# Performance work log

Hardware: AMD Instinct MI355X
Metric: run time of the kernel (lower is better)

Reference implementation:

```python
import jax, jax.numpy as jnp
import numpy as np

B, N, D, S, ITERS = 32, 4096, 256, 7, 3
EPS_LN = 1e-5

def _ln(x, g, b):
    m = jnp.mean(x, axis=-1, keepdims=True)
    v = jnp.mean((x - m) ** 2, axis=-1, keepdims=True)
    return g * (x - m) * jax.lax.rsqrt(v + EPS_LN) + b

def setup_inputs() -> dict:
    key = jax.random.key(0)
    ks = jax.random.split(key, 16)
    w = lambda k, shape: (jax.random.normal(k, shape, jnp.float32) * 0.02)
    return {
        "inputs": jax.random.normal(ks[0], (B, N, D), jnp.float32),
        "noise": jax.random.normal(ks[1], (B, S, D), jnp.float32),
        "ln_in_g": jnp.ones((D,), jnp.float32), "ln_in_b": jnp.zeros((D,), jnp.float32),
        "ln_slots_g": jnp.ones((D,), jnp.float32), "ln_slots_b": jnp.zeros((D,), jnp.float32),
        "ln_mlp_g": jnp.ones((D,), jnp.float32), "ln_mlp_b": jnp.zeros((D,), jnp.float32),
        "slots_mu": w(ks[2], (1, 1, D)),
        "slots_sigma": jnp.ones((1, 1, D), jnp.float32),
        "wq": w(ks[3], (D, D)), "bq": jnp.zeros((D,), jnp.float32),
        "wk": w(ks[4], (D, D)), "bk": jnp.zeros((D,), jnp.float32),
        "wv": w(ks[5], (D, D)), "bv": jnp.zeros((D,), jnp.float32),
        "w_ih": w(ks[6], (3 * D, D)), "b_ih": jnp.zeros((3 * D,), jnp.float32),
        "w_hh": w(ks[7], (3 * D, D)), "b_hh": jnp.zeros((3 * D,), jnp.float32),
        "w1": w(ks[8], (2 * D, D)), "b1": jnp.zeros((2 * D,), jnp.float32),
        "w2": w(ks[9], (D, 2 * D)), "b2": jnp.zeros((D,), jnp.float32),
    }

def reference(inputs, noise, ln_in_g, ln_in_b, ln_slots_g, ln_slots_b, ln_mlp_g, ln_mlp_b,
              slots_mu, slots_sigma, wq, bq, wk, bk, wv, bv,
              w_ih, b_ih, w_hh, b_hh, w1, b1, w2, b2):
    x = _ln(inputs, ln_in_g, ln_in_b)                      # [B,N,D]
    sigma = jax.nn.softplus(slots_sigma)
    slots = slots_mu + sigma * noise                       # [B,S,D]
    k = x @ wk.T + bk                                      # [B,N,D]
    v = x @ wv.T + bv                                      # [B,N,D]
    scale = D ** -0.5
    attn = None
    for _ in range(ITERS):
        slots_prev = slots
        q = _ln(slots, ln_slots_g, ln_slots_b) @ wq.T + bq  # [B,S,D]
        logits = jnp.einsum('bsd,bnd->bsn', q, k) * scale   # [B,S,N]
        attn = jax.nn.softmax(logits, axis=1) + 1e-8        # softmax over slots
        attn = attn / jnp.sum(attn, axis=-1, keepdims=True)
        updates = jnp.einsum('bsn,bnd->bsd', attn, v)       # [B,S,D]
        # GRUCell(updates, slots_prev), torch gate order (r, z, n)
        gi = updates @ w_ih.T + b_ih                        # [B,S,3D]
        gh = slots_prev @ w_hh.T + b_hh
        i_r, i_z, i_n = jnp.split(gi, 3, axis=-1)
        h_r, h_z, h_n = jnp.split(gh, 3, axis=-1)
        r = jax.nn.sigmoid(i_r + h_r)
        z = jax.nn.sigmoid(i_z + h_z)
        n = jnp.tanh(i_n + r * h_n)
        slots = (1.0 - z) * n + z * slots_prev
        h = jax.nn.relu(_ln(slots, ln_mlp_g, ln_mlp_b) @ w1.T + b1)
        slots = slots + h @ w2.T + b2
    return slots, jnp.swapaxes(attn, 1, 2)                 # [B,S,D], [B,N,S]
```

## Files before the change

kernel.cpp:

```cpp
#include <hip/hip_runtime.h>
#include <stdint.h>

typedef unsigned short u16;
typedef unsigned int u32;
typedef float f32x4 __attribute__((ext_vector_type(4)));
typedef short short8 __attribute__((ext_vector_type(8)));

#define NBAT 32
#define NSEQ 4096
#define ND 256
#define NSLOT 7
#define NCHUNK 64

__device__ __forceinline__ u32 bf16rne(float f){
  u32 u = __float_as_uint(f);
  u = u + 0x7FFFu + ((u >> 16) & 1u);
  return u >> 16;
}
__device__ __forceinline__ u32 packbf(float a, float b){
  return (bf16rne(a) & 0xFFFFu) | (bf16rne(b) << 16);
}
__device__ __forceinline__ float bflo(u32 u){ return __uint_as_float(u << 16); }
__device__ __forceinline__ float bfhi(u32 u){ return __uint_as_float(u & 0xFFFF0000u); }

__device__ __forceinline__ void gld16(void* lds, const void* g){
  __builtin_amdgcn_global_load_lds(
      (const __attribute__((address_space(1))) u32*)g,
      (__attribute__((address_space(3))) u32*)lds, 16, 0, 0);
}

__device__ __forceinline__ void softmax7(const float* z, float* p){
  float m = fmaxf(fmaxf(fmaxf(z[0], z[1]), fmaxf(z[2], z[3])),
                  fmaxf(fmaxf(z[4], z[5]), z[6]));
  float sum = 0.f;
#pragma unroll
  for (int s = 0; s < 7; ++s){ p[s] = exp2f(z[s] - m); sum += p[s]; }
  float r = 1.f / sum;
#pragma unroll
  for (int s = 0; s < 7; ++s) p[s] = fmaf(p[s], r, 1e-8f);
}

__global__ __launch_bounds__(256) void k_prep(
    const float* __restrict__ wk, const float* __restrict__ wv,
    const float* __restrict__ bk, const float* __restrict__ bv,
    const float* __restrict__ mu, const float* __restrict__ sig,
    const float* __restrict__ noise,
    const float* __restrict__ w_ih, const float* __restrict__ b_ih,
    const float* __restrict__ w_hh, const float* __restrict__ b_hh,
    const float* __restrict__ w1, const float* __restrict__ w2,
    const float* __restrict__ wq,
    u16* __restrict__ Wkv, float* __restrict__ biaskv, float* __restrict__ slots,
    u16* __restrict__ Wg, u16* __restrict__ w1b, u16* __restrict__ w2b,
    u16* __restrict__ wqb, float* __restrict__ bg){
  const int bid = blockIdx.x, t = threadIdx.x;
  if (bid < 512){
    const float* src = (bid < 256) ? (wk + (size_t)bid*256) : (wv + (size_t)(bid-256)*256);
    Wkv[(size_t)bid*256 + t] = (u16)bf16rne(src[t]);
  } else if (bid == 512){
    biaskv[t] = bk[t];
    biaskv[256 + t] = bv[t];
  } else if (bid < 737){
    int r = bid - 513;
    float sp = logf(1.f + expf(sig[t]));
    slots[(size_t)r*256 + t] = mu[t] + sp * noise[(size_t)r*256 + t];
  } else if (bid < 1761){
    int j = bid - 737;
    u16 a, b;
    if (j < 512){ a = (u16)bf16rne(w_ih[(size_t)j*256 + t]); b = (u16)bf16rne(w_hh[(size_t)j*256 + t]); }
    else if (j < 768){ a = (u16)bf16rne(w_ih[(size_t)j*256 + t]); b = 0; }
    else { a = 0; b = (u16)bf16rne(w_hh[(size_t)(j-256)*256 + t]); }
    Wg[(size_t)j*512 + t] = a;
    Wg[(size_t)j*512 + 256 + t] = b;
  } else if (bid < 2273){
    int j = bid - 1761;
    w1b[(size_t)j*256 + t] = (u16)bf16rne(w1[(size_t)j*256 + t]);
  } else if (bid < 2529){
    int j = bid - 2273;
    w2b[(size_t)j*512 + t]       = (u16)bf16rne(w2[(size_t)j*512 + t]);
    w2b[(size_t)j*512 + 256 + t] = (u16)bf16rne(w2[(size_t)j*512 + 256 + t]);
  } else if (bid < 2785){
    int j = bid - 2529;
    wqb[(size_t)j*256 + t] = (u16)bf16rne(wq[(size_t)j*256 + t]);
  } else {
#pragma unroll
    for (int ii = 0; ii < 4; ++ii){
      int j = ii*256 + t;
      float v;
      if (j < 512) v = b_ih[j] + b_hh[j];
      else if (j < 768) v = b_ih[j];
      else v = b_hh[j - 256];
      bg[j] = v;
    }
  }
}

__global__ __launch_bounds__(256) void k_ln_in(
    const float* __restrict__ x, const float* __restrict__ g, const float* __restrict__ b,
    u16* __restrict__ xo){
  const int row = blockIdx.x*4 + (threadIdx.x >> 6);
  const int lane = threadIdx.x & 63;
  const f32x4 v = *(const f32x4*)(x + (size_t)row*ND + lane*4);
  float s  = v[0]+v[1]+v[2]+v[3];
  float s2 = v[0]*v[0]+v[1]*v[1]+v[2]*v[2]+v[3]*v[3];
#pragma unroll
  for (int m = 1; m < 64; m <<= 1){ s += __shfl_xor(s, m); s2 += __shfl_xor(s2, m); }
  const float mean = s * (1.f/256.f);
  const float var  = s2 * (1.f/256.f) - mean*mean;
  const float rstd = rsqrtf(var + 1e-5f);
  const f32x4 gg = *(const f32x4*)(g + lane*4);
  const f32x4 bb = *(const f32x4*)(b + lane*4);
  float y0 = (v[0]-mean)*rstd*gg[0] + bb[0];
  float y1 = (v[1]-mean)*rstd*gg[1] + bb[1];
  float y2 = (v[2]-mean)*rstd*gg[2] + bb[2];
  float y3 = (v[3]-mean)*rstd*gg[3] + bb[3];
  uint2 o; o.x = packbf(y0, y1); o.y = packbf(y2, y3);
  *(uint2*)(xo + (size_t)row*ND + lane*4) = o;
}

__global__ __launch_bounds__(256) void k_gemm_kv(
    const u16* __restrict__ X, const u16* __restrict__ W,
    const float* __restrict__ biaskv, u16* __restrict__ kv){
  __shared__ __align__(16) u16 At[128*64];
  __shared__ __align__(16) u16 Bt[128*64];
  const int bid = blockIdx.x;
  const int swz = ((bid & 7) << 9) + (bid >> 3);
  const int mb = swz >> 2, nb = swz & 3;
  const int tid = threadIdx.x, w = tid >> 6, lane = tid & 63;
  const int wm = w >> 1, wn = w & 1;
  f32x4 acc[4][4];
#pragma unroll
  for (int a = 0; a < 4; ++a)
#pragma unroll
    for (int c = 0; c < 4; ++c) acc[a][c] = (f32x4){0.f,0.f,0.f,0.f};

  const int cl = lane & 7;
  for (int kt = 0; kt < 4; ++kt){
#pragma unroll
    for (int i = 0; i < 4; ++i){
      int R = w*32 + i*8 + (lane >> 3);
      int c = cl ^ (R & 7);
      gld16(&At[(w*32 + i*8)*64], X + ((size_t)(mb*128 + R))*256 + kt*64 + c*8);
      gld16(&Bt[(w*32 + i*8)*64], W + ((size_t)(nb*128 + R))*256 + kt*64 + c*8);
    }
    __syncthreads();
#pragma unroll
    for (int kk = 0; kk < 2; ++kk){
      short8 xf[4], wf[4];
#pragma unroll
      for (int xi = 0; xi < 4; ++xi){
        int r = wm*64 + xi*16 + (lane & 15);
        int ch = (kk*4 + (lane >> 4)) ^ (r & 7);
        xf[xi] = *(const short8*)&At[r*64 + ch*8];
      }
#pragma unroll
      for (int wi = 0; wi < 4; ++wi){
        int r = wn*64 + wi*16 + (lane & 15);
        int ch = (kk*4 + (lane >> 4)) ^ (r & 7);
        wf[wi] = *(const short8*)&Bt[r*64 + ch*8];
      }
#pragma unroll
      for (int xi = 0; xi < 4; ++xi)
#pragma unroll
        for (int wi = 0; wi < 4; ++wi)
          acc[xi][wi] = __builtin_amdgcn_mfma_f32_16x16x32_bf16(wf[wi], xf[xi], acc[xi][wi], 0, 0, 0);
    }
    __syncthreads();
  }
  f32x4 bias[4];
#pragma unroll
  for (int wi = 0; wi < 4; ++wi)
    bias[wi] = *(const f32x4*)(biaskv + nb*128 + wn*64 + wi*16 + (lane >> 4)*4);
#pragma unroll
  for (int xi = 0; xi < 4; ++xi){
    size_t m = (size_t)mb*128 + wm*64 + xi*16 + (lane & 15);
    u16* dst = kv + m*512 + nb*128 + wn*64 + (lane >> 4)*4;
#pragma unroll
    for (int wi = 0; wi < 4; ++wi){
      f32x4 c = acc[xi][wi];
      uint2 o;
      o.x = packbf(c[0] + bias[wi][0], c[1] + bias[wi][1]);
      o.y = packbf(c[2] + bias[wi][2], c[3] + bias[wi][3]);
      *(uint2*)(dst + wi*16) = o;
    }
  }
}

template<int MODE>
__global__ __launch_bounds__(256) void k_gemm_s(
    const u16* __restrict__ A, const u16* __restrict__ W,
    const float* __restrict__ bias, int nkt,
    float* __restrict__ outf, u16* __restrict__ outb,
    const float* __restrict__ snew, float* __restrict__ out2, int last){
  __shared__ __align__(16) u16 At[128*64];
  __shared__ __align__(16) u16 Bt[128*64];
  const int nb = blockIdx.x, mb = blockIdx.y;
  const int tid = threadIdx.x, w = tid >> 6, lane = tid & 63;
  const int wm = w >> 1, wn = w & 1;
  const size_t K = (size_t)nkt * 64;
  f32x4 acc[4][4];
#pragma unroll
  for (int a = 0; a < 4; ++a)
#pragma unroll
    for (int c = 0; c < 4; ++c) acc[a][c] = (f32x4){0.f,0.f,0.f,0.f};

  const int cl = lane & 7;
  for (int kt = 0; kt < nkt; ++kt){
#pragma unroll
    for (int i = 0; i < 4; ++i){
      int R = w*32 + i*8 + (lane >> 3);
      int c = cl ^ (R & 7);
      gld16(&At[(w*32 + i*8)*64], A + ((size_t)(mb*128 + R))*K + kt*64 + c*8);
      gld16(&Bt[(w*32 + i*8)*64], W + ((size_t)(nb*128 + R))*K + kt*64 + c*8);
    }
    __syncthreads();
#pragma unroll
    for (int kk = 0; kk < 2; ++kk){
      short8 xf[4], wf[4];
#pragma unroll
      for (int xi = 0; xi < 4; ++xi){
        int r = wm*64 + xi*16 + (lane & 15);
        int ch = (kk*4 + (lane >> 4)) ^ (r & 7);
        xf[xi] = *(const short8*)&At[r*64 + ch*8];
      }
#pragma unroll
      for (int wi = 0; wi < 4; ++wi){
        int r = wn*64 + wi*16 + (lane & 15);
        int ch = (kk*4 + (lane >> 4)) ^ (r & 7);
        wf[wi] = *(const short8*)&Bt[r*64 + ch*8];
      }
#pragma unroll
      for (int xi = 0; xi < 4; ++xi)
#pragma unroll
        for (int wi = 0; wi < 4; ++wi)
          acc[xi][wi] = __builtin_amdgcn_mfma_f32_16x16x32_bf16(wf[wi], xf[xi], acc[xi][wi], 0, 0, 0);
    }
    __syncthreads();
  }
  const int LDO = (MODE == 0) ? 1024 : ((MODE == 1) ? 512 : 256);
  f32x4 b4[4];
#pragma unroll
  for (int wi = 0; wi < 4; ++wi)
    b4[wi] = *(const f32x4*)(bias + nb*128 + wn*64 + wi*16 + (lane >> 4)*4);
#pragma unroll
  for (int xi = 0; xi < 4; ++xi){
    const int m = mb*128 + wm*64 + xi*16 + (lane & 15);
    const int colb = nb*128 + wn*64 + (lane >> 4)*4;
#pragma unroll
    for (int wi = 0; wi < 4; ++wi){
      const int col = colb + wi*16;
      f32x4 c = acc[xi][wi] + b4[wi];
      if (MODE == 0){
        *(f32x4*)(outf + (size_t)m*LDO + col) = c;
      } else if (MODE == 1){
        uint2 o;
        o.x = packbf(fmaxf(c[0],0.f), fmaxf(c[1],0.f));
        o.y = packbf(fmaxf(c[2],0.f), fmaxf(c[3],0.f));
        *(uint2*)(outb + (size_t)m*LDO + col) = o;
      } else if (MODE == 2){
        if (m < 224){
          const f32x4 s4 = *(const f32x4*)(snew + (size_t)m*256 + col);
          f32x4 o = c + s4;
          *(f32x4*)(outf + (size_t)m*LDO + col) = o;
          if (last) *(f32x4*)(out2 + (size_t)m*LDO + col) = o;
        }
      } else {
        f32x4 o = c * 0.09016844f;
        *(f32x4*)(outf + (size_t)m*LDO + col) = o;
      }
    }
  }
}

__global__ __launch_bounds__(256) void k_attn(
    const u16* __restrict__ kv, const float* __restrict__ qeff,
    float* __restrict__ attn_out, float* __restrict__ pacc, float* __restrict__ pw){
  __shared__ __align__(16) float accbuf[4][7][256];
  __shared__ float wsbuf[4][7];
  const int chunk = blockIdx.x, b = blockIdx.y;
  const int tid = threadIdx.x, w = tid >> 6, lane = tid & 63, hi = lane >> 5, lo = lane & 31;
  float qr[7][8];
  {
    const float* qb = qeff + (size_t)b*(NSLOT*256) + lo*8;
#pragma unroll
    for (int s = 0; s < 7; ++s){
      f32x4 q0 = *(const f32x4*)(qb + s*256);
      f32x4 q1 = *(const f32x4*)(qb + s*256 + 4);
      qr[s][0]=q0[0]; qr[s][1]=q0[1]; qr[s][2]=q0[2]; qr[s][3]=q0[3];
      qr[s][4]=q1[0]; qr[s][5]=q1[1]; qr[s][6]=q1[2]; qr[s][7]=q1[3];
    }
  }
  float acc[7][4]; float wsm[7];
#pragma unroll
  for (int s = 0; s < 7; ++s){ acc[s][0]=acc[s][1]=acc[s][2]=acc[s][3]=0.f; wsm[s]=0.f; }

  const size_t bbase = (size_t)b*NSEQ;
  const int nr0 = chunk*64 + w*2;
  uint4 k4; uint2 va, vb;
  {
    const size_t rowm = (bbase + nr0 + hi)*512;
    const size_t rowo = (bbase + nr0 + (1 - hi))*512;
    k4 = *(const uint4*)(kv + rowm + lo*8);
    va = *(const uint2*)(kv + rowm + 256 + (size_t)lane*4);
    vb = *(const uint2*)(kv + rowo + 256 + (size_t)lane*4);
  }
  for (int it = 0; it < 8; ++it){
    const int nr = nr0 + it*8;
    uint4 k4n; uint2 van, vbn;
    if (it < 7){
      const size_t rowmn = (bbase + nr + 8 + hi)*512;
      const size_t rowon = (bbase + nr + 8 + (1 - hi))*512;
      k4n = *(const uint4*)(kv + rowmn + lo*8);
      van = *(const uint2*)(kv + rowmn + 256 + (size_t)lane*4);
      vbn = *(const uint2*)(kv + rowon + 256 + (size_t)lane*4);
    }
    float kf[8];
    kf[0]=bflo(k4.x); kf[1]=bfhi(k4.x); kf[2]=bflo(k4.y); kf[3]=bfhi(k4.y);
    kf[4]=bflo(k4.z); kf[5]=bfhi(k4.z); kf[6]=bflo(k4.w); kf[7]=bfhi(k4.w);
    float z[7];
#pragma unroll
    for (int s = 0; s < 7; ++s){
      float d0 = fmaf(qr[s][0],kf[0], fmaf(qr[s][1],kf[1], fmaf(qr[s][2],kf[2], qr[s][3]*kf[3])));
      float d1 = fmaf(qr[s][4],kf[4], fmaf(qr[s][5],kf[5], fmaf(qr[s][6],kf[6], qr[s][7]*kf[7])));
      z[s] = d0 + d1;
    }
#pragma unroll
    for (int m = 1; m < 32; m <<= 1){
#pragma unroll
      for (int s = 0; s < 7; ++s) z[s] += __shfl_xor(z[s], m);
    }
    float zo[7];
#pragma unroll
    for (int s = 0; s < 7; ++s) zo[s] = __shfl_xor(z[s], 32);
    float pm[7], po[7];
    softmax7(z, pm);
    softmax7(zo, po);
    float sel = pm[0];
    sel = (lo==1)?pm[1]:sel; sel = (lo==2)?pm[2]:sel; sel = (lo==3)?pm[3]:sel;
    sel = (lo==4)?pm[4]:sel; sel = (lo==5)?pm[5]:sel; sel = (lo==6)?pm[6]:sel;
    if (lo < 7) attn_out[((size_t)bbase + nr + hi)*7 + lo] = sel;
    float vm0=bflo(va.x), vm1=bfhi(va.x), vm2=bflo(va.y), vm3=bfhi(va.y);
    float vo0=bflo(vb.x), vo1=bfhi(vb.x), vo2=bflo(vb.y), vo3=bfhi(vb.y);
#pragma unroll
    for (int s = 0; s < 7; ++s){
      acc[s][0] = fmaf(pm[s], vm0, fmaf(po[s], vo0, acc[s][0]));
      acc[s][1] = fmaf(pm[s], vm1, fmaf(po[s], vo1, acc[s][1]));
      acc[s][2] = fmaf(pm[s], vm2, fmaf(po[s], vo2, acc[s][2]));
      acc[s][3] = fmaf(pm[s], vm3, fmaf(po[s], vo3, acc[s][3]));
      wsm[s] += pm[s] + po[s];
    }
    if (it < 7){ k4 = k4n; va = van; vb = vbn; }
  }
#pragma unroll
  for (int s = 0; s < 7; ++s)
    *(f32x4*)&accbuf[w][s][lane*4] = (f32x4){acc[s][0], acc[s][1], acc[s][2], acc[s][3]};
  if (lane == 0){
#pragma unroll
    for (int s = 0; s < 7; ++s) wsbuf[w][s] = wsm[s];
  }
  __syncthreads();
#pragma unroll
  for (int s = 0; s < 7; ++s){
    float sum = accbuf[0][s][tid] + accbuf[1][s][tid] + accbuf[2][s][tid] + accbuf[3][s][tid];
    pacc[((size_t)chunk*NBAT + b)*(NSLOT*256) + s*256 + tid] = sum;
  }
  if (tid < 7)
    pw[((size_t)chunk*NBAT + b)*NSLOT + tid] =
        wsbuf[0][tid] + wsbuf[1][tid] + wsbuf[2][tid] + wsbuf[3][tid];
}

__global__ __launch_bounds__(256) void k_slotA(
    const float* __restrict__ pacc, const float* __restrict__ pw,
    const float* __restrict__ slots, u16* __restrict__ A2, float* __restrict__ wsum){
  __shared__ float pwb[NCHUNK];
  const int r = blockIdx.x, t = threadIdx.x;
  if (r >= 224){
    A2[(size_t)r*512 + t] = 0;
    A2[(size_t)r*512 + 256 + t] = 0;
    return;
  }
  if (t < NCHUNK) pwb[t] = pw[(size_t)t*224 + r];
  float u = 0.f;
#pragma unroll 8
  for (int c = 0; c < NCHUNK; ++c) u += pacc[(size_t)c*57344 + (size_t)r*256 + t];
  __syncthreads();
  float wst = 0.f;
#pragma unroll
  for (int c = 0; c < NCHUNK; ++c) wst += pwb[c];
  if (t == 0) wsum[r] = wst;
  A2[(size_t)r*512 + t] = (u16)bf16rne(u / wst);
  A2[(size_t)r*512 + 256 + t] = (u16)bf16rne(slots[(size_t)r*256 + t]);
}

__global__ __launch_bounds__(256) void k_slotB(
    const float* __restrict__ gates, const float* __restrict__ slots,
    const float* __restrict__ gm, const float* __restrict__ bm,
    float* __restrict__ snew, u16* __restrict__ lnm){
  __shared__ float red[8];
  const int r = blockIdx.x, t = threadIdx.x;
  if (r >= 224){ lnm[(size_t)r*256 + t] = 0; return; }
  const float g0  = gates[(size_t)r*1024 + t];
  const float g1  = gates[(size_t)r*1024 + 256 + t];
  const float gin = gates[(size_t)r*1024 + 512 + t];
  const float ghn = gates[(size_t)r*1024 + 768 + t];
  const float spv = slots[(size_t)r*256 + t];
  const float rr = 1.f/(1.f + __expf(-g0));
  const float zz = 1.f/(1.f + __expf(-g1));
  float xx = gin + rr*ghn;
  xx = fminf(fmaxf(xx, -15.f), 15.f);
  const float e2 = __expf(2.f*xx);
  const float nn = (e2 - 1.f)/(e2 + 1.f);
  const float sp = (1.f - zz)*nn + zz*spv;
  snew[(size_t)r*256 + t] = sp;
  float s = sp, s2 = sp*sp;
#pragma unroll
  for (int m = 1; m < 64; m <<= 1){ s += __shfl_xor(s, m); s2 += __shfl_xor(s2, m); }
  if ((t & 63) == 0){ red[t >> 6] = s; red[4 + (t >> 6)] = s2; }
  __syncthreads();
  const float ssum = red[0]+red[1]+red[2]+red[3];
  const float qsum = red[4]+red[5]+red[6]+red[7];
  const float mean = ssum*(1.f/256.f);
  const float var  = qsum*(1.f/256.f) - mean*mean;
  const float rstd = rsqrtf(var + 1e-5f);
  lnm[(size_t)r*256 + t] = (u16)bf16rne((sp - mean)*rstd*gm[t] + bm[t]);
}

__global__ __launch_bounds__(256) void k_lnq(
    const float* __restrict__ slots, const float* __restrict__ g, const float* __restrict__ b,
    u16* __restrict__ lnq){
  __shared__ float red[8];
  const int r = blockIdx.x, t = threadIdx.x;
  if (r >= 224){ lnq[(size_t)r*256 + t] = 0; return; }
  const float x = slots[(size_t)r*256 + t];
  float s = x, s2 = x*x;
#pragma unroll
  for (int m = 1; m < 64; m <<= 1){ s += __shfl_xor(s, m); s2 += __shfl_xor(s2, m); }
  if ((t & 63) == 0){ red[t >> 6] = s; red[4 + (t >> 6)] = s2; }
  __syncthreads();
  const float ssum = red[0]+red[1]+red[2]+red[3];
  const float qsum = red[4]+red[5]+red[6]+red[7];
  const float mean = ssum*(1.f/256.f);
  const float var  = qsum*(1.f/256.f) - mean*mean;
  const float rstd = rsqrtf(var + 1e-5f);
  lnq[(size_t)r*256 + t] = (u16)bf16rne((x - mean)*rstd*g[t] + b[t]);
}

__global__ __launch_bounds__(256) void k_norm(
    float* __restrict__ attn, const float* __restrict__ wsum_tot){
  size_t i = (size_t)blockIdx.x*256 + threadIdx.x;
  int s = (int)(i % 7);
  int b = (int)(i / (NSEQ*7));
  attn[i] = attn[i] / wsum_tot[b*7 + s];
}

extern "C" void kernel_launch(void* const* d_in, const int* in_sizes, int n_in,
                              void* d_out, int out_size, void* d_ws, size_t ws_size,
                              hipStream_t stream){
  (void)in_sizes; (void)n_in; (void)out_size; (void)ws_size;
  const float* inputs  = (const float*)d_in[0];
  const float* noise   = (const float*)d_in[1];
  const float* ln_in_g = (const float*)d_in[2];
  const float* ln_in_b = (const float*)d_in[3];
  const float* ln_sl_g = (const float*)d_in[4];
  const float* ln_sl_b = (const float*)d_in[5];
  const float* ln_ml_g = (const float*)d_in[6];
  const float* ln_ml_b = (const float*)d_in[7];
  const float* mu      = (const float*)d_in[8];
  const float* sig     = (const float*)d_in[9];
  const float* wq      = (const float*)d_in[10];
  const float* bq      = (const float*)d_in[11];
  const float* wk      = (const float*)d_in[12];
  const float* bk      = (const float*)d_in[13];
  const float* wv      = (const float*)d_in[14];
  const float* bv      = (const float*)d_in[15];
  const float* w_ih    = (const float*)d_in[16];
  const float* b_ih    = (const float*)d_in[17];
  const float* w_hh    = (const float*)d_in[18];
  const float* b_hh    = (const float*)d_in[19];
  const float* w1      = (const float*)d_in[20];
  const float* b1      = (const float*)d_in[21];
  const float* w2      = (const float*)d_in[22];
  const float* b2      = (const float*)d_in[23];

  char* ws = (char*)d_ws;
  u16*   x_bf   = (u16*)(ws);
  u16*   kv     = (u16*)(ws + 67108864);
  char*  paccch = ws + 201326592;
  float* pacc   = (float*)paccch;
  u16*   Wkv    = (u16*)(ws + 216006656);
  float* qeff   = (float*)(ws + 216268800);
  float* slots  = (float*)(ws + 216530944);
  float* pw     = (float*)(ws + 216760320);
  float* biaskv = (float*)(ws + 216817664);
  float* wsum   = (float*)(ws + 216819712);
  u16*   A2     = (u16*)(ws + 216820736);
  u16*   Wg     = (u16*)(ws + 217082880);
  u16*   w1b    = (u16*)(ws + 218131456);
  u16*   w2b    = (u16*)(ws + 218393600);
  u16*   wqb    = (u16*)(ws + 218655744);
  float* bg     = (float*)(ws + 218786816);

  float* gates  = (float*)(paccch);
  u16*   hb     = (u16*)(paccch + 1048576);
  u16*   lnm    = (u16*)(paccch + 1310720);
  u16*   lnq    = (u16*)(paccch + 1441792);
  float* snew   = (float*)(paccch + 1572864);

  float* out_slots = (float*)d_out;
  float* attn = (float*)d_out + 57344;

  k_prep<<<2786, 256, 0, stream>>>(wk, wv, bk, bv, mu, sig, noise,
                                   w_ih, b_ih, w_hh, b_hh, w1, w2, wq,
                                   Wkv, biaskv, slots, Wg, w1b, w2b, wqb, bg);
  k_ln_in<<<32768, 256, 0, stream>>>(inputs, ln_in_g, ln_in_b, x_bf);
  k_gemm_kv<<<4096, 256, 0, stream>>>(x_bf, Wkv, biaskv, kv);
  for (int i = 0; i < 3; ++i){
    const int last = (i == 2) ? 1 : 0;
    k_lnq<<<256, 256, 0, stream>>>(slots, ln_sl_g, ln_sl_b, lnq);
    k_gemm_s<3><<<dim3(2, 2), 256, 0, stream>>>(lnq, wqb, bq, 4, qeff, nullptr, nullptr, nullptr, 0);
    k_attn<<<dim3(NCHUNK, 32), 256, 0, stream>>>(kv, qeff, attn, pacc, pw);
    k_slotA<<<256, 256, 0, stream>>>(pacc, pw, slots, A2, wsum);
    k_gemm_s<0><<<dim3(8, 2), 256, 0, stream>>>(A2, Wg, bg, 8, gates, nullptr, nullptr, nullptr, 0);
    k_slotB<<<256, 256, 0, stream>>>(gates, slots, ln_ml_g, ln_ml_b, snew, lnm);
    k_gemm_s<1><<<dim3(4, 2), 256, 0, stream>>>(lnm, w1b, b1, 4, nullptr, hb, nullptr, nullptr, 0);
    k_gemm_s<2><<<dim3(2, 2), 256, 0, stream>>>(hb, w2b, b2, 8, slots, nullptr, snew, out_slots, last);
  }
  k_norm<<<3584, 256, 0, stream>>>(attn, wsum);
}
```

Before: 417.2 us.

## Compute slot attention logits with MFMA and double-buffer GEMM LDS tiles

```diff
diff --git a/kernel.cpp b/kernel.cpp
--- a/kernel.cpp
+++ b/kernel.cpp
@@ -27,17 +27,6 @@
   __builtin_amdgcn_global_load_lds(
       (const __attribute__((address_space(1))) u32*)g,
       (__attribute__((address_space(3))) u32*)lds, 16, 0, 0);
-}
-
-__device__ __forceinline__ void softmax7(const float* z, float* p){
-  float m = fmaxf(fmaxf(fmaxf(z[0], z[1]), fmaxf(z[2], z[3])),
-                  fmaxf(fmaxf(z[4], z[5]), z[6]));
-  float sum = 0.f;
-#pragma unroll
-  for (int s = 0; s < 7; ++s){ p[s] = exp2f(z[s] - m); sum += p[s]; }
-  float r = 1.f / sum;
-#pragma unroll
-  for (int s = 0; s < 7; ++s) p[s] = fmaf(p[s], r, 1e-8f);
 }
 
 __global__ __launch_bounds__(256) void k_prep(
@@ -120,8 +109,8 @@
 __global__ __launch_bounds__(256) void k_gemm_kv(
     const u16* __restrict__ X, const u16* __restrict__ W,
     const float* __restrict__ biaskv, u16* __restrict__ kv){
-  __shared__ __align__(16) u16 At[128*64];
-  __shared__ __align__(16) u16 Bt[128*64];
+  __shared__ __align__(16) u16 At[2][128*64];
+  __shared__ __align__(16) u16 Bt[2][128*64];
   const int bid = blockIdx.x;
   const int swz = ((bid & 7) << 9) + (bid >> 3);
   const int mb = swz >> 2, nb = swz & 3;
@@ -134,15 +123,21 @@
     for (int c = 0; c < 4; ++c) acc[a][c] = (f32x4){0.f,0.f,0.f,0.f};
 
   const int cl = lane & 7;
+#define STAGE_KV(buf, kt)                                                        \
+  {                                                                              \
+    _Pragma("unroll")                                                            \
+    for (int i = 0; i < 4; ++i){                                                 \
+      int R = w*32 + i*8 + (lane >> 3);                                          \
+      int c = cl ^ (R & 7);                                                      \
+      gld16(&At[buf][(w*32 + i*8)*64], X + ((size_t)(mb*128 + R))*256 + (kt)*64 + c*8); \
+      gld16(&Bt[buf][(w*32 + i*8)*64], W + ((size_t)(nb*128 + R))*256 + (kt)*64 + c*8); \
+    }                                                                            \
+  }
+  STAGE_KV(0, 0);
+  __syncthreads();
   for (int kt = 0; kt < 4; ++kt){
-#pragma unroll
-    for (int i = 0; i < 4; ++i){
-      int R = w*32 + i*8 + (lane >> 3);
-      int c = cl ^ (R & 7);
-      gld16(&At[(w*32 + i*8)*64], X + ((size_t)(mb*128 + R))*256 + kt*64 + c*8);
-      gld16(&Bt[(w*32 + i*8)*64], W + ((size_t)(nb*128 + R))*256 + kt*64 + c*8);
-    }
-    __syncthreads();
+    const int cur = kt & 1;
+    if (kt < 3) STAGE_KV(cur ^ 1, kt + 1);
 #pragma unroll
     for (int kk = 0; kk < 2; ++kk){
       short8 xf[4], wf[4];
@@ -150,13 +145,13 @@
       for (int xi = 0; xi < 4; ++xi){
         int r = wm*64 + xi*16 + (lane & 15);
         int ch = (kk*4 + (lane >> 4)) ^ (r & 7);
-        xf[xi] = *(const short8*)&At[r*64 + ch*8];
+        xf[xi] = *(const short8*)&At[cur][r*64 + ch*8];
       }
 #pragma unroll
       for (int wi = 0; wi < 4; ++wi){
         int r = wn*64 + wi*16 + (lane & 15);
         int ch = (kk*4 + (lane >> 4)) ^ (r & 7);
-        wf[wi] = *(const short8*)&Bt[r*64 + ch*8];
+        wf[wi] = *(const short8*)&Bt[cur][r*64 + ch*8];
       }
 #pragma unroll
       for (int xi = 0; xi < 4; ++xi)
@@ -166,6 +161,7 @@
     }
     __syncthreads();
   }
+#undef STAGE_KV
   f32x4 bias[4];
 #pragma unroll
   for (int wi = 0; wi < 4; ++wi)
@@ -191,8 +187,8 @@
     const float* __restrict__ bias, int nkt,
     float* __restrict__ outf, u16* __restrict__ outb,
     const float* __restrict__ snew, float* __restrict__ out2, int last){
-  __shared__ __align__(16) u16 At[128*64];
-  __shared__ __align__(16) u16 Bt[128*64];
+  __shared__ __align__(16) u16 At[2][128*64];
+  __shared__ __align__(16) u16 Bt[2][128*64];
   const int nb = blockIdx.x, mb = blockIdx.y;
   const int tid = threadIdx.x, w = tid >> 6, lane = tid & 63;
   const int wm = w >> 1, wn = w & 1;
@@ -204,15 +200,21 @@
     for (int c = 0; c < 4; ++c) acc[a][c] = (f32x4){0.f,0.f,0.f,0.f};
 
   const int cl = lane & 7;
+#define STAGE_S(buf, kt)                                                         \
+  {                                                                              \
+    _Pragma("unroll")                                                            \
+    for (int i = 0; i < 4; ++i){                                                 \
+      int R = w*32 + i*8 + (lane >> 3);                                          \
+      int c = cl ^ (R & 7);                                                      \
+      gld16(&At[buf][(w*32 + i*8)*64], A + ((size_t)(mb*128 + R))*K + (kt)*64 + c*8); \
+      gld16(&Bt[buf][(w*32 + i*8)*64], W + ((size_t)(nb*128 + R))*K + (kt)*64 + c*8); \
+    }                                                                            \
+  }
+  STAGE_S(0, 0);
+  __syncthreads();
   for (int kt = 0; kt < nkt; ++kt){
-#pragma unroll
-    for (int i = 0; i < 4; ++i){
-      int R = w*32 + i*8 + (lane >> 3);
-      int c = cl ^ (R & 7);
-      gld16(&At[(w*32 + i*8)*64], A + ((size_t)(mb*128 + R))*K + kt*64 + c*8);
-      gld16(&Bt[(w*32 + i*8)*64], W + ((size_t)(nb*128 + R))*K + kt*64 + c*8);
-    }
-    __syncthreads();
+    const int cur = kt & 1;
+    if (kt < nkt - 1) STAGE_S(cur ^ 1, kt + 1);
 #pragma unroll
     for (int kk = 0; kk < 2; ++kk){
       short8 xf[4], wf[4];
@@ -220,13 +222,13 @@
       for (int xi = 0; xi < 4; ++xi){
         int r = wm*64 + xi*16 + (lane & 15);
         int ch = (kk*4 + (lane >> 4)) ^ (r & 7);
-        xf[xi] = *(const short8*)&At[r*64 + ch*8];
+        xf[xi] = *(const short8*)&At[cur][r*64 + ch*8];
       }
 #pragma unroll
       for (int wi = 0; wi < 4; ++wi){
         int r = wn*64 + wi*16 + (lane & 15);
         int ch = (kk*4 + (lane >> 4)) ^ (r & 7);
-        wf[wi] = *(const short8*)&Bt[r*64 + ch*8];
+        wf[wi] = *(const short8*)&Bt[cur][r*64 + ch*8];
       }
 #pragma unroll
       for (int xi = 0; xi < 4; ++xi)
@@ -236,6 +238,7 @@
     }
     __syncthreads();
   }
+#undef STAGE_S
   const int LDO = (MODE == 0) ? 1024 : ((MODE == 1) ? 512 : 256);
   f32x4 b4[4];
 #pragma unroll
@@ -264,99 +267,103 @@
           if (last) *(f32x4*)(out2 + (size_t)m*LDO + col) = o;
         }
       } else {
-        f32x4 o = c * 0.09016844f;
-        *(f32x4*)(outf + (size_t)m*LDO + col) = o;
+        uint2 o;
+        o.x = packbf(c[0]*0.09016844f, c[1]*0.09016844f);
+        o.y = packbf(c[2]*0.09016844f, c[3]*0.09016844f);
+        *(uint2*)(outb + (size_t)m*LDO + col) = o;
       }
     }
   }
 }
 
 __global__ __launch_bounds__(256) void k_attn(
-    const u16* __restrict__ kv, const float* __restrict__ qeff,
+    const u16* __restrict__ kv, const u16* __restrict__ qb,
     float* __restrict__ attn_out, float* __restrict__ pacc, float* __restrict__ pw){
   __shared__ __align__(16) float accbuf[4][7][256];
-  __shared__ float wsbuf[4][7];
+  __shared__ __align__(16) float p_lds[4][16][8];
+  __shared__ float wsum_lds[4][8];
   const int chunk = blockIdx.x, b = blockIdx.y;
-  const int tid = threadIdx.x, w = tid >> 6, lane = tid & 63, hi = lane >> 5, lo = lane & 31;
-  float qr[7][8];
+  const int tid = threadIdx.x, w = tid >> 6, lane = tid & 63;
+  const int l15 = lane & 15, g = lane >> 4, hi = lane >> 5;
+  const size_t bbase = (size_t)b*NSEQ;
+  const int nr0 = chunk*64 + w*16;
+
+  short8 qf[8];
   {
-    const float* qb = qeff + (size_t)b*(NSLOT*256) + lo*8;
-#pragma unroll
-    for (int s = 0; s < 7; ++s){
-      f32x4 q0 = *(const f32x4*)(qb + s*256);
-      f32x4 q1 = *(const f32x4*)(qb + s*256 + 4);
-      qr[s][0]=q0[0]; qr[s][1]=q0[1]; qr[s][2]=q0[2]; qr[s][3]=q0[3];
-      qr[s][4]=q1[0]; qr[s][5]=q1[1]; qr[s][6]=q1[2]; qr[s][7]=q1[3];
-    }
-  }
-  float acc[7][4]; float wsm[7];
-#pragma unroll
-  for (int s = 0; s < 7; ++s){ acc[s][0]=acc[s][1]=acc[s][2]=acc[s][3]=0.f; wsm[s]=0.f; }
-
-  const size_t bbase = (size_t)b*NSEQ;
-  const int nr0 = chunk*64 + w*2;
-  uint4 k4; uint2 va, vb;
-  {
-    const size_t rowm = (bbase + nr0 + hi)*512;
-    const size_t rowo = (bbase + nr0 + (1 - hi))*512;
-    k4 = *(const uint4*)(kv + rowm + lo*8);
-    va = *(const uint2*)(kv + rowm + 256 + (size_t)lane*4);
-    vb = *(const uint2*)(kv + rowo + 256 + (size_t)lane*4);
-  }
+    const u16* qrow = qb + ((size_t)b*7 + l15)*256;
+#pragma unroll
+    for (int ks = 0; ks < 8; ++ks)
+      qf[ks] = *(const short8*)(qrow + (ks*4 + g)*8);
+  }
+  f32x4 z = {0.f,0.f,0.f,0.f};
+#pragma unroll
+  for (int ks = 0; ks < 8; ++ks){
+    const short8 kf = *(const short8*)(kv + (bbase + nr0 + l15)*512 + (ks*4 + g)*8);
+    z = __builtin_amdgcn_mfma_f32_16x16x32_bf16(qf[ks], kf, z, 0, 0, 0);
+  }
+  float zz[4];
+#pragma unroll
+  for (int j = 0; j < 4; ++j){
+    const int s = g*4 + j;
+    zz[j] = (s < 7) ? z[j] : -3.0e38f;
+  }
+  float mx = fmaxf(fmaxf(zz[0], zz[1]), fmaxf(zz[2], zz[3]));
+  mx = fmaxf(mx, __shfl_xor(mx, 16));
+  float p[4], psum = 0.f;
+#pragma unroll
+  for (int j = 0; j < 4; ++j){ p[j] = exp2f(zz[j] - mx); psum += p[j]; }
+  psum += __shfl_xor(psum, 16);
+  const float rs = 1.f / psum;
+#pragma unroll
+  for (int j = 0; j < 4; ++j) p[j] = fmaf(p[j], rs, 1e-8f);
+  float wloc[4] = {0.f,0.f,0.f,0.f};
+  if (lane < 32){
+    *(f32x4*)&p_lds[w][l15][g*4] = (f32x4){p[0], p[1], p[2], p[3]};
+    const size_t arow = (bbase + nr0 + l15)*7;
+#pragma unroll
+    for (int j = 0; j < 4; ++j){
+      const int s = g*4 + j;
+      if (s < 7){ attn_out[arow + s] = p[j]; wloc[j] = p[j]; }
+    }
+  }
+  __syncthreads();
+  float acc[7][4];
+#pragma unroll
+  for (int s = 0; s < 7; ++s){ acc[s][0]=acc[s][1]=acc[s][2]=acc[s][3]=0.f; }
+#pragma unroll
   for (int it = 0; it < 8; ++it){
-    const int nr = nr0 + it*8;
-    uint4 k4n; uint2 van, vbn;
-    if (it < 7){
-      const size_t rowmn = (bbase + nr + 8 + hi)*512;
-      const size_t rowon = (bbase + nr + 8 + (1 - hi))*512;
-      k4n = *(const uint4*)(kv + rowmn + lo*8);
-      van = *(const uint2*)(kv + rowmn + 256 + (size_t)lane*4);
-      vbn = *(const uint2*)(kv + rowon + 256 + (size_t)lane*4);
-    }
-    float kf[8];
-    kf[0]=bflo(k4.x); kf[1]=bfhi(k4.x); kf[2]=bflo(k4.y); kf[3]=bfhi(k4.y);
-    kf[4]=bflo(k4.z); kf[5]=bfhi(k4.z); kf[6]=bflo(k4.w); kf[7]=bfhi(k4.w);
-    float z[7];
-#pragma unroll
-    for (int s = 0; s < 7; ++s){
-      float d0 = fmaf(qr[s][0],kf[0], fmaf(qr[s][1],kf[1], fmaf(qr[s][2],kf[2], qr[s][3]*kf[3])));
-      float d1 = fmaf(qr[s][4],kf[4], fmaf(qr[s][5],kf[5], fmaf(qr[s][6],kf[6], qr[s][7]*kf[7])));
-      z[s] = d0 + d1;
-    }
-#pragma unroll
-    for (int m = 1; m < 32; m <<= 1){
-#pragma unroll
-      for (int s = 0; s < 7; ++s) z[s] += __shfl_xor(z[s], m);
-    }
-    float zo[7];
-#pragma unroll
-    for (int s = 0; s < 7; ++s) zo[s] = __shfl_xor(z[s], 32);
-    float pm[7], po[7];
-    softmax7(z, pm);
-    softmax7(zo, po);
-    float sel = pm[0];
-    sel = (lo==1)?pm[1]:sel; sel = (lo==2)?pm[2]:sel; sel = (lo==3)?pm[3]:sel;
-    sel = (lo==4)?pm[4]:sel; sel = (lo==5)?pm[5]:sel; sel = (lo==6)?pm[6]:sel;
-    if (lo < 7) attn_out[((size_t)bbase + nr + hi)*7 + lo] = sel;
-    float vm0=bflo(va.x), vm1=bfhi(va.x), vm2=bflo(va.y), vm3=bfhi(va.y);
-    float vo0=bflo(vb.x), vo1=bfhi(vb.x), vo2=bflo(vb.y), vo3=bfhi(vb.y);
+    const int rm = it*2 + hi, ro = it*2 + (1 - hi);
+    const uint2 va = *(const uint2*)(kv + (bbase + nr0 + rm)*512 + 256 + (size_t)lane*4);
+    const uint2 vb = *(const uint2*)(kv + (bbase + nr0 + ro)*512 + 256 + (size_t)lane*4);
+    const f32x4 pm0 = *(const f32x4*)&p_lds[w][rm][0];
+    const f32x4 pm1 = *(const f32x4*)&p_lds[w][rm][4];
+    const f32x4 po0 = *(const f32x4*)&p_lds[w][ro][0];
+    const f32x4 po1 = *(const f32x4*)&p_lds[w][ro][4];
+    const float pm[7] = {pm0[0],pm0[1],pm0[2],pm0[3],pm1[0],pm1[1],pm1[2]};
+    const float po[7] = {po0[0],po0[1],po0[2],po0[3],po1[0],po1[1],po1[2]};
+    const float vm0=bflo(va.x), vm1=bfhi(va.x), vm2=bflo(va.y), vm3=bfhi(va.y);
+    const float vo0=bflo(vb.x), vo1=bfhi(vb.x), vo2=bflo(vb.y), vo3=bfhi(vb.y);
 #pragma unroll
     for (int s = 0; s < 7; ++s){
       acc[s][0] = fmaf(pm[s], vm0, fmaf(po[s], vo0, acc[s][0]));
       acc[s][1] = fmaf(pm[s], vm1, fmaf(po[s], vo1, acc[s][1]));
       acc[s][2] = fmaf(pm[s], vm2, fmaf(po[s], vo2, acc[s][2]));
       acc[s][3] = fmaf(pm[s], vm3, fmaf(po[s], vo3, acc[s][3]));
-      wsm[s] += pm[s] + po[s];
-    }
-    if (it < 7){ k4 = k4n; va = van; vb = vbn; }
-  }
+    }
+  }
+#pragma unroll
+  for (int m = 1; m < 16; m <<= 1){
+#pragma unroll
+    for (int j = 0; j < 4; ++j) wloc[j] += __shfl_xor(wloc[j], m);
+  }
+  if (lane < 32 && l15 == 0){
+#pragma unroll
+    for (int j = 0; j < 4; ++j) wsum_lds[w][g*4 + j] = wloc[j];
+  }
+  __syncthreads();
 #pragma unroll
   for (int s = 0; s < 7; ++s)
     *(f32x4*)&accbuf[w][s][lane*4] = (f32x4){acc[s][0], acc[s][1], acc[s][2], acc[s][3]};
-  if (lane == 0){
-#pragma unroll
-    for (int s = 0; s < 7; ++s) wsbuf[w][s] = wsm[s];
-  }
   __syncthreads();
 #pragma unroll
   for (int s = 0; s < 7; ++s){
@@ -365,7 +372,7 @@
   }
   if (tid < 7)
     pw[((size_t)chunk*NBAT + b)*NSLOT + tid] =
-        wsbuf[0][tid] + wsbuf[1][tid] + wsbuf[2][tid] + wsbuf[3][tid];
+        wsum_lds[0][tid] + wsum_lds[1][tid] + wsum_lds[2][tid] + wsum_lds[3][tid];
 }
 
 __global__ __launch_bounds__(256) void k_slotA(
@@ -487,7 +494,7 @@
   char*  paccch = ws + 201326592;
   float* pacc   = (float*)paccch;
   u16*   Wkv    = (u16*)(ws + 216006656);
-  float* qeff   = (float*)(ws + 216268800);
+  u16*   qeffb  = (u16*)(ws + 216268800);
   float* slots  = (float*)(ws + 216530944);
   float* pw     = (float*)(ws + 216760320);
   float* biaskv = (float*)(ws + 216817664);
@@ -516,8 +523,8 @@
   for (int i = 0; i < 3; ++i){
     const int last = (i == 2) ? 1 : 0;
     k_lnq<<<256, 256, 0, stream>>>(slots, ln_sl_g, ln_sl_b, lnq);
-    k_gemm_s<3><<<dim3(2, 2), 256, 0, stream>>>(lnq, wqb, bq, 4, qeff, nullptr, nullptr, nullptr, 0);
-    k_attn<<<dim3(NCHUNK, 32), 256, 0, stream>>>(kv, qeff, attn, pacc, pw);
+    k_gemm_s<3><<<dim3(2, 2), 256, 0, stream>>>(lnq, wqb, bq, 4, nullptr, qeffb, nullptr, nullptr, 0);
+    k_attn<<<dim3(NCHUNK, 32), 256, 0, stream>>>(kv, qeffb, attn, pacc, pw);
     k_slotA<<<256, 256, 0, stream>>>(pacc, pw, slots, A2, wsum);
     k_gemm_s<0><<<dim3(8, 2), 256, 0, stream>>>(A2, Wg, bg, 8, gates, nullptr, nullptr, nullptr, 0);
     k_slotB<<<256, 256, 0, stream>>>(gates, slots, ln_ml_g, ln_ml_b, snew, lnm);
```

Result: faster. 373.3 us (-10.5%).
